# Optimization experiments

Measured on AMD Instinct MI355X. Metric: run time of the kernel, lower is better.

## Reference

```python
import jax, jax.numpy as jnp
import numpy as np

B, S, D = 16, 4096, 64
N_HASHES = 8
BUCKET_SIZE = 64
N_BUCKETS = S // BUCKET_SIZE  # 64
NEG = -5e4  # the module uses -50000.0 as masking value
EPS = 1e-6


def setup_inputs() -> dict:
    key = jax.random.key(0)
    k1, k2, k3 = jax.random.split(key, 3)
    qk = jax.random.normal(k1, (B, S, D), dtype=jnp.float32)
    v = jax.random.normal(k2, (B, S, D), dtype=jnp.float32)
    # random rotations for LSH: (batch, dim, n_hashes, n_buckets//2)
    rotations = jax.random.normal(k3, (B, D, N_HASHES, N_BUCKETS // 2), dtype=jnp.float32)
    return {"qk": qk, "v": v, "rotations": rotations, "seed_": 0}


def _look_one_back(x):
    # prepend previous chunk (with wraparound) along the key axis
    x_extra = jnp.concatenate([x[:, -1:], x[:, :-1]], axis=1)
    return jnp.concatenate([x, x_extra], axis=2)


def reference(qk, v, rotations, seed_):
    b, s, d = qk.shape
    n_hashes = rotations.shape[2]
    n_buckets = 2 * rotations.shape[3]
    chunks = n_hashes * n_buckets  # n_bins == n_buckets

    # ---- hash_vectors ----
    rot = jnp.einsum('btf,bfhi->bhti', qk, rotations)          # (b, h, s, nb/2)
    rot = jnp.concatenate([rot, -rot], axis=-1)                # (b, h, s, nb)
    buckets = jnp.argmax(rot, axis=-1)                         # (b, h, s)
    offsets = (jnp.arange(n_hashes) * n_buckets)[None, :, None]
    buckets = (buckets + offsets).reshape(b, n_hashes * s)     # (b, h*s)

    # ---- sort by (bucket, position) ----
    ticker = jnp.arange(n_hashes * s)
    buckets_and_t = s * buckets + (ticker % s)[None, :]
    sticker = jnp.argsort(buckets_and_t, axis=-1)              # stable sort indices
    undo_sort = jnp.argsort(sticker, axis=-1)

    st = sticker % s                                           # original positions
    sqk = jnp.take_along_axis(qk, st[..., None], axis=1)       # (b, h*s, d)
    sv = jnp.take_along_axis(v, st[..., None], axis=1)

    bq_t = st.reshape(b, chunks, -1)                           # (b, chunks, bucket)
    bqk = sqk.reshape(b, chunks, -1, d)
    bv = sv.reshape(b, chunks, -1, d)

    bq = bqk
    norm = jnp.linalg.norm(bqk, axis=-1, keepdims=True)
    bk = bqk / (norm + EPS)                                    # make_unit_length

    bk = _look_one_back(bk)                                    # (b, chunks, 2*bucket, d)
    bv = _look_one_back(bv)
    bkv_t = _look_one_back(bq_t[..., None])[..., 0]            # (b, chunks, 2*bucket)

    dots = jnp.einsum('bhie,bhje->bhij', bq, bk) * (d ** -0.5)
    self_mask = bq_t[:, :, :, None] == bkv_t[:, :, None, :]
    dots = jnp.where(self_mask, NEG, dots)

    dots_lse = jax.nn.logsumexp(dots, axis=-1, keepdims=True)  # (b, chunks, bucket, 1)
    probs = jnp.exp(dots - dots_lse)
    bo = jnp.einsum('buij,buje->buie', probs, bv)              # (b, chunks, bucket, d)

    so = bo.reshape(b, n_hashes * s, d)
    slogits = dots_lse.reshape(b, n_hashes * s)

    # ---- unsort ----
    o = jnp.take_along_axis(so, undo_sort[..., None], axis=1)
    logits = jnp.take_along_axis(slogits, undo_sort, axis=-1)

    # ---- combine hash rounds via logsumexp weights ----
    o = o.reshape(b, n_hashes, s, d)
    logits = logits.reshape(b, n_hashes, s, 1)
    w = jnp.exp(logits - jax.nn.logsumexp(logits, axis=1, keepdims=True))
    out = jnp.sum(o * w, axis=1)                               # (b, s, d)
    return out, buckets
```

## Files before the change

### kernel.cpp

```cpp
#include <hip/hip_runtime.h>
#include <math.h>

#define BB   16
#define SS   4096
#define DD   64
#define HH   8
#define NBH  32
#define NB   64
#define NCH  512

typedef __attribute__((ext_vector_type(8))) short s16x8;
typedef __attribute__((ext_vector_type(4))) short s16x4;
typedef __attribute__((ext_vector_type(4))) float f32x4;
typedef __attribute__((ext_vector_type(4))) unsigned u32x4;

static __device__ __forceinline__ unsigned short f2bf(float x) {
  union { float f; unsigned u; } a; a.f = x;
  unsigned r = a.u + 0x7fffu + ((a.u >> 16) & 1u);
  return (unsigned short)(r >> 16);
}
static __device__ __forceinline__ float bf2f(unsigned short u) {
  union { unsigned u; float f; } a; a.u = ((unsigned)u) << 16;
  return a.f;
}
static __device__ __forceinline__ unsigned bfrnd_hi(float x) {
  union { float f; unsigned u; } a; a.f = x;
  return a.u + 0x7fffu + ((a.u >> 16) & 1u);
}
static __device__ __forceinline__ unsigned pack_bf(float lo, float hi) {
  return __builtin_amdgcn_perm(bfrnd_hi(hi), bfrnd_hi(lo), 0x07060302u);
}

__global__ __launch_bounds__(256) void k_conv(
    const float* __restrict__ qk, const float* __restrict__ v,
    unsigned short* __restrict__ qb, unsigned short* __restrict__ kb,
    unsigned short* __restrict__ vb) {
  const int gid = blockIdx.x * 256 + threadIdx.x;
  const int half = BB * SS * 4;
  const bool isV = gid >= half;
  const int id = isV ? gid - half : gid;
  const int row = id >> 2, q4 = id & 3;

  const float4* src =
      (const float4*)((isV ? v : qk) + (size_t)row * DD + q4 * 16);
  float vals[16];
#pragma unroll
  for (int g = 0; g < 4; g++) {
    const float4 a = src[g];
    vals[g * 4 + 0] = a.x; vals[g * 4 + 1] = a.y;
    vals[g * 4 + 2] = a.z; vals[g * 4 + 3] = a.w;
  }

  if (!isV) {
    float ss = 0.f;
#pragma unroll
    for (int i = 0; i < 16; i++) ss += vals[i] * vals[i];
    ss += __shfl_xor(ss, 1);
    ss += __shfl_xor(ss, 2);
    const float scl = 0.125f / (sqrtf(ss) + 1e-6f);
    unsigned short qo[16], ko[16];
#pragma unroll
    for (int i = 0; i < 16; i++) {
      qo[i] = f2bf(vals[i]);
      ko[i] = f2bf(vals[i] * scl);
    }
    unsigned short* qd = qb + (size_t)row * DD + q4 * 16;
    unsigned short* kd = kb + (size_t)row * DD + q4 * 16;
    *(s16x8*)qd = *(const s16x8*)&qo[0];
    *(s16x8*)(qd + 8) = *(const s16x8*)&qo[8];
    *(s16x8*)kd = *(const s16x8*)&ko[0];
    *(s16x8*)(kd + 8) = *(const s16x8*)&ko[8];
  } else {
    unsigned short vo[16];
#pragma unroll
    for (int i = 0; i < 16; i++) vo[i] = f2bf(vals[i]);
    unsigned short* vd = vb + (size_t)row * DD + q4 * 16;
    *(s16x8*)vd = *(const s16x8*)&vo[0];
    *(s16x8*)(vd + 8) = *(const s16x8*)&vo[8];
  }
}

__global__ __launch_bounds__(256) void k_rotT(
    const float* __restrict__ rot, unsigned short* __restrict__ rTh,
    unsigned short* __restrict__ rTl, int* __restrict__ needy_count) {
  __shared__ float slab[32][256];
  const int b = blockIdx.x;
  const int tid = threadIdx.x;
  if (b == 0 && tid == 0) *needy_count = 0;

  for (int st = 0; st < 2; st++) {
#pragma unroll
    for (int fr = 0; fr < 32; fr++)
      slab[fr][tid] = rot[(size_t)b * (DD * HH * NBH) +
                          (size_t)(st * 32 + fr) * 256 + tid];
    __syncthreads();
    unsigned short hi[32], lo[32];
#pragma unroll
    for (int fr = 0; fr < 32; fr++) {
      const float x = slab[fr][tid];
      const unsigned short hh = f2bf(x);
      hi[fr] = hh;
      lo[fr] = f2bf(x - bf2f(hh));
    }
    unsigned short* dh = rTh + ((size_t)b * 256 + tid) * DD + st * 32;
    unsigned short* dl = rTl + ((size_t)b * 256 + tid) * DD + st * 32;
#pragma unroll
    for (int g = 0; g < 4; g++) {
      *(s16x8*)(dh + g * 8) = *(const s16x8*)&hi[g * 8];
      *(s16x8*)(dl + g * 8) = *(const s16x8*)&lo[g * 8];
    }
    __syncthreads();
  }
}

#define MARGIN 1e-2f

__global__ __launch_bounds__(256, 4) void k_hash_mfma(
    const float* __restrict__ qk, const unsigned short* __restrict__ rTh,
    const unsigned short* __restrict__ rTl, int* __restrict__ bucket_local,
    float* __restrict__ buckets_out, int* __restrict__ needy_list,
    int* __restrict__ needy_count) {
  __shared__ struct __align__(16) {
    unsigned short ah[64][72];
    unsigned short al[64][72];
    float sc[2][64][33];
  } sm;
  const int b = blockIdx.x;
  const int t0 = blockIdx.y * 64;
  const int tid = threadIdx.x;
  const int w = tid >> 6, lane = tid & 63;
  const int quad = lane >> 4, l16 = lane & 15;

  {
    const int row = tid >> 2, qf = tid & 3;
    const float4* src =
        (const float4*)(qk + ((size_t)b * SS + t0 + row) * DD + qf * 16);
#pragma unroll
    for (int gg = 0; gg < 2; gg++) {
      const float4 v0 = src[gg * 2], v1 = src[gg * 2 + 1];
      const float a[8] = {v0.x, v0.y, v0.z, v0.w, v1.x, v1.y, v1.z, v1.w};
      unsigned short hi[8], lo[8];
#pragma unroll
      for (int e = 0; e < 8; e++) {
        const unsigned short hh = f2bf(a[e]);
        hi[e] = hh;
        lo[e] = f2bf(a[e] - bf2f(hh));
      }
      *(s16x8*)&sm.ah[row][qf * 16 + gg * 8] = *(const s16x8*)hi;
      *(s16x8*)&sm.al[row][qf * 16 + gg * 8] = *(const s16x8*)lo;
    }
  }
  __syncthreads();

  s16x8 Ah[2], Al[2];
#pragma unroll
  for (int ks = 0; ks < 2; ks++) {
    Ah[ks] = *(const s16x8*)&sm.ah[w * 16 + l16][ks * 32 + quad * 8];
    Al[ks] = *(const s16x8*)&sm.al[w * 16 + l16][ks * 32 + quad * 8];
  }

#pragma unroll 1
  for (int h = 0; h < HH; h++) {
    const int p = h & 1;
#pragma unroll
    for (int nt = 0; nt < 2; nt++) {
      const size_t rrow = (((size_t)b * HH + h) * 32 + nt * 16 + l16) * DD;
      s16x8 Bh2[2], Bl2[2];
#pragma unroll
      for (int ks = 0; ks < 2; ks++) {
        Bh2[ks] = *(const s16x8*)&rTh[rrow + ks * 32 + quad * 8];
        Bl2[ks] = *(const s16x8*)&rTl[rrow + ks * 32 + quad * 8];
      }
      f32x4 acc = (f32x4){0.f, 0.f, 0.f, 0.f};
#pragma unroll
      for (int ks = 0; ks < 2; ks++) {
        acc = __builtin_amdgcn_mfma_f32_16x16x32_bf16(Al[ks], Bl2[ks], acc, 0, 0, 0);
        acc = __builtin_amdgcn_mfma_f32_16x16x32_bf16(Al[ks], Bh2[ks], acc, 0, 0, 0);
        acc = __builtin_amdgcn_mfma_f32_16x16x32_bf16(Ah[ks], Bl2[ks], acc, 0, 0, 0);
        acc = __builtin_amdgcn_mfma_f32_16x16x32_bf16(Ah[ks], Bh2[ks], acc, 0, 0, 0);
      }
#pragma unroll
      for (int r = 0; r < 4; r++)
        sm.sc[p][w * 16 + quad * 4 + r][nt * 16 + l16] = acc[r];
    }
    __syncthreads();

    {
      const int tloc = w * 16 + l16;
      const float sgn = (quad >= 2) ? -1.0f : 1.0f;
      const float* rowp = &sm.sc[p][tloc][(quad & 1) * 16];
      float best = -3.0e38f, second = -3.0e38f;
      int bi = quad * 16;
#pragma unroll 8
      for (int i = 0; i < 16; i++) {
        const float vv = sgn * rowp[i];
        if (vv > best) { second = best; best = vv; bi = quad * 16 + i; }
        else if (vv > second) second = vv;
      }
      {
        const float ob = __shfl_xor(best, 16);
        const float os = __shfl_xor(second, 16);
        const int obi = __shfl_xor(bi, 16);
        const float ms = fmaxf(fminf(best, ob), fmaxf(second, os));
        const bool partnerLower = (lane & 16) != 0;
        if (partnerLower ? (ob >= best) : (ob > best)) { best = ob; bi = obi; }
        second = ms;
      }
      {
        const float ob = __shfl_xor(best, 32);
        const float os = __shfl_xor(second, 32);
        const int obi = __shfl_xor(bi, 32);
        const float ms = fmaxf(fminf(best, ob), fmaxf(second, os));
        const bool partnerLower = (lane & 32) != 0;
        if (partnerLower ? (ob >= best) : (ob > best)) { best = ob; bi = obi; }
        second = ms;
      }
      if (quad == 0) {
        const int t = t0 + tloc;
        bucket_local[((size_t)b * HH + h) * SS + t] = bi;
        buckets_out[(size_t)b * (HH * SS) + (size_t)h * SS + t] =
            (float)(h * NB + bi);
        if (best - second <= MARGIN) {
          const int slot = atomicAdd(needy_count, 1);
          needy_list[slot] = (((b << 3) | h) << 12) | t;
        }
      }
    }
  }
}

__global__ __launch_bounds__(256) void k_hash_fix(
    const float* __restrict__ qk, const float* __restrict__ rot,
    const int* __restrict__ needy_list, const int* __restrict__ needy_count,
    int* __restrict__ bucket_local, float* __restrict__ buckets_out) {
  const int n = *needy_count;
  const int hw = (blockIdx.x * 256 + (int)threadIdx.x) >> 5;
  const int li = threadIdx.x & 31;
  const int nhw = gridDim.x * 8;

  for (int idx = hw; idx < n; idx += nhw) {
    const int code = needy_list[idx];
    const int t = code & 4095;
    const int bh = code >> 12;
    const int b = bh >> 3, h = bh & 7;

    const float* qrow = qk + ((size_t)b * SS + t) * DD;
    const float* rcol = rot + ((size_t)b * DD * HH + h) * NBH + li;

    double acc = 0.0;
#pragma unroll 8
    for (int f = 0; f < DD; f++)
      acc += (double)qrow[f] * (double)rcol[(size_t)f * (HH * NBH)];

    double bv = acc;
    int bi = li;
    if (-acc > bv) { bv = -acc; bi = li + 32; }
#pragma unroll
    for (int off = 1; off < 32; off <<= 1) {
      const double ov = __shfl_xor(bv, off);
      const int oi = __shfl_xor(bi, off);
      if (ov > bv || (ov == bv && oi < bi)) { bv = ov; bi = oi; }
    }
    if (li == 0) {
      bucket_local[((size_t)b * HH + h) * SS + t] = bi;
      buckets_out[(size_t)b * (HH * SS) + (size_t)h * SS + t] =
          (float)(h * NB + bi);
    }
  }
}

__global__ __launch_bounds__(256) void k_sort(
    const int* __restrict__ bucket_local, int* __restrict__ sort_t,
    int* __restrict__ ipos) {
  __shared__ unsigned short lb[SS];
  __shared__ unsigned char  cnt[NB][256];
  __shared__ unsigned short pfx[NB][256];
  __shared__ int part[NB][4];
  __shared__ int tot[NB];
  __shared__ int base[NB];

  const int bh = blockIdx.x;
  const int tid = threadIdx.x;
  const int* src = bucket_local + (size_t)bh * SS;

  int* czero = (int*)&cnt[0][0];
#pragma unroll
  for (int i = 0; i < 16; i++) czero[tid + i * 256] = 0;
  __syncthreads();

#pragma unroll
  for (int i = 0; i < 16; i++) {
    const int t = tid * 16 + i;
    const int v = src[t];
    lb[t] = (unsigned short)v;
    cnt[v][tid]++;
  }
  __syncthreads();

  {
    const int bk = tid & 63, sg = tid >> 6;
    int s = 0;
#pragma unroll 8
    for (int i = 0; i < 64; i++) s += cnt[bk][sg * 64 + i];
    part[bk][sg] = s;
  }
  __syncthreads();
  if (tid < NB) tot[tid] = part[tid][0] + part[tid][1] + part[tid][2] + part[tid][3];
  __syncthreads();
  if (tid == 0) {
    int r = 0;
    for (int i = 0; i < NB; i++) { base[i] = r; r += tot[i]; }
  }
  __syncthreads();
  {
    const int bk = tid & 63, sg = tid >> 6;
    int run = base[bk];
    for (int s = 0; s < sg; s++) run += part[bk][s];
#pragma unroll 8
    for (int i = 0; i < 64; i++) {
      const int th = sg * 64 + i;
      pfx[bk][th] = (unsigned short)run;
      run += cnt[bk][th];
    }
  }
  __syncthreads();
  int* st = sort_t + (size_t)bh * SS;
#pragma unroll
  for (int i = 0; i < 16; i++) {
    const int t = tid * 16 + i;
    const int bk = lb[t];
    const int pos = pfx[bk][tid]++;
    st[pos] = t;
  }
  (void)ipos;
}

__global__ __launch_bounds__(256, 4) void k_attn2(
    const unsigned short* __restrict__ qb, const unsigned short* __restrict__ kbg,
    const unsigned short* __restrict__ vbg, const int* __restrict__ sort_t,
    unsigned short* __restrict__ so, float* __restrict__ lse_u) {
  const int blk = blockIdx.x;
  const int b = blk >> 9;
  const int c = blk & 511;
  const int h = c >> 6, cc = c & 63;
  const int cp = (c + 511) & 511;
  const int hp = cp >> 6, ccp = cp & 63;

  __shared__ struct __align__(16) {
    union {
      unsigned short kb[128][72];
      unsigned short p[64][136];
      float olds[64][68];
    } kp;
    unsigned short vsT[64][136];
    int tk[128];
  } sm;

  const int tid = threadIdx.x;
  const int w = tid >> 6;
  const int lane = tid & 63;
  const int quad = lane >> 4;
  const int l16 = lane & 15;

  if (tid < 128) {
    const size_t srci = (tid < 64)
        ? (((size_t)b * HH + h) * SS + cc * 64 + tid)
        : (((size_t)b * HH + hp) * SS + ccp * 64 + (tid - 64));
    sm.tk[tid] = sort_t[srci];
  }
  __syncthreads();

  {
    const int j = tid >> 1, hf = tid & 1;
    const int trow = sm.tk[j];
    const s16x8* ksrc = (const s16x8*)(kbg + ((size_t)b * SS + trow) * DD + hf * 32);
    s16x8 kr[4];
#pragma unroll
    for (int g = 0; g < 4; g++) kr[g] = ksrc[g];
#pragma unroll
    for (int g = 0; g < 4; g++)
      *(s16x8*)&sm.kp.kb[j][hf * 32 + g * 8] = kr[g];
  }
  {
    const int fg = tid >> 5;
    const int tg = (tid & 31) << 2;
    const unsigned short* vb_b = vbg + (size_t)b * SS * DD + fg * 8;
    const u32x4 a0v = *(const u32x4*)(vb_b + (size_t)sm.tk[tg + 0] * DD);
    const u32x4 a1v = *(const u32x4*)(vb_b + (size_t)sm.tk[tg + 1] * DD);
    const u32x4 a2v = *(const u32x4*)(vb_b + (size_t)sm.tk[tg + 2] * DD);
    const u32x4 a3v = *(const u32x4*)(vb_b + (size_t)sm.tk[tg + 3] * DD);
#pragma unroll
    for (int j = 0; j < 4; j++) {
      uint2 ev, ov;
      ev.x = __builtin_amdgcn_perm(a1v[j], a0v[j], 0x05040100u);
      ev.y = __builtin_amdgcn_perm(a3v[j], a2v[j], 0x05040100u);
      ov.x = __builtin_amdgcn_perm(a1v[j], a0v[j], 0x07060302u);
      ov.y = __builtin_amdgcn_perm(a3v[j], a2v[j], 0x07060302u);
      *(uint2*)&sm.vsT[fg * 8 + 2 * j][tg] = ev;
      *(uint2*)&sm.vsT[fg * 8 + 2 * j + 1][tg] = ov;
    }
  }
  const int tq = sm.tk[w * 16 + l16];
  const unsigned short* qrowp = qb + ((size_t)b * SS + tq) * DD;
  const s16x8 a0 = *(const s16x8*)(qrowp + quad * 8);
  const s16x8 a1 = *(const s16x8*)(qrowp + 32 + quad * 8);
  __syncthreads();

  f32x4 acc[8];
#pragma unroll
  for (int nt = 0; nt < 8; nt++) acc[nt] = (f32x4){0.f, 0.f, 0.f, 0.f};
#pragma unroll
  for (int nt = 0; nt < 8; nt++) {
    const s16x8 b0 = *(const s16x8*)&sm.kp.kb[nt * 16 + l16][quad * 8];
    const s16x8 b1 = *(const s16x8*)&sm.kp.kb[nt * 16 + l16][32 + quad * 8];
    acc[nt] = __builtin_amdgcn_mfma_f32_16x16x32_bf16(b0, a0, acc[nt], 0, 0, 0);
    acc[nt] = __builtin_amdgcn_mfma_f32_16x16x32_bf16(b1, a1, acc[nt], 0, 0, 0);
  }

  {
    const bool dm = (quad == (l16 >> 2));
    const int rm = l16 & 3;
#pragma unroll
    for (int nt = 0; nt < 4; nt++)
      if (nt == w) {
#pragma unroll
        for (int r = 0; r < 4; r++)
          if (dm && rm == r) acc[nt][r] = -50000.0f;
      }
  }
  if (cc == 0) {
#pragma unroll
    for (int nt = 4; nt < 8; nt++)
#pragma unroll
      for (int r = 0; r < 4; r++)
        if (sm.tk[nt * 16 + quad * 4 + r] == tq) acc[nt][r] = -50000.0f;
  }

  float mv[8];
#pragma unroll
  for (int nt = 0; nt < 8; nt++)
    mv[nt] = fmaxf(fmaxf(acc[nt][0], acc[nt][1]), fmaxf(acc[nt][2], acc[nt][3]));
  float m = fmaxf(fmaxf(fmaxf(mv[0], mv[1]), fmaxf(mv[2], mv[3])),
                  fmaxf(fmaxf(mv[4], mv[5]), fmaxf(mv[6], mv[7])));
  m = fmaxf(m, __shfl_xor(m, 16));
  m = fmaxf(m, __shfl_xor(m, 32));

  float sv[8];
#pragma unroll
  for (int nt = 0; nt < 8; nt++) {
#pragma unroll
    for (int r = 0; r < 4; r++) acc[nt][r] = __expf(acc[nt][r] - m);
    sv[nt] = (acc[nt][0] + acc[nt][1]) + (acc[nt][2] + acc[nt][3]);
  }
  float s = ((sv[0] + sv[1]) + (sv[2] + sv[3])) +
            ((sv[4] + sv[5]) + (sv[6] + sv[7]));
  s += __shfl_xor(s, 16);
  s += __shfl_xor(s, 32);
  const float inv = 1.0f / s;
  const float lse = __logf(s) + m;

  if (quad == 0)
    lse_u[((size_t)b * SS + tq) * HH + h] = lse;

  __syncthreads();

  {
    const int prow = w * 16 + l16;
#pragma unroll
    for (int nt = 0; nt < 8; nt++) {
      uint2 pv;
      pv.x = pack_bf(acc[nt][0] * inv, acc[nt][1] * inv);
      pv.y = pack_bf(acc[nt][2] * inv, acc[nt][3] * inv);
      *(uint2*)&sm.kp.p[prow][nt * 16 + quad * 4] = pv;
    }
  }
  __syncthreads();

  f32x4 o[4];
#pragma unroll
  for (int nt = 0; nt < 4; nt++) o[nt] = (f32x4){0.f, 0.f, 0.f, 0.f};
  const unsigned short* vrow = &sm.vsT[w * 16 + l16][0];
#pragma unroll
  for (int kc = 0; kc < 4; kc++) {
    const s16x8 av = *(const s16x8*)(vrow + kc * 32 + quad * 8);
#pragma unroll
    for (int nt = 0; nt < 4; nt++) {
      const s16x8 bp = *(const s16x8*)&sm.kp.p[nt * 16 + l16][kc * 32 + quad * 8];
      o[nt] = __builtin_amdgcn_mfma_f32_16x16x32_bf16(av, bp, o[nt], 0, 0, 0);
    }
  }

  __syncthreads();

#pragma unroll
  for (int nt = 0; nt < 4; nt++)
    *(f32x4*)&sm.kp.olds[nt * 16 + l16][w * 16 + quad * 4] = o[nt];
  __syncthreads();

  {
    const int q = tid >> 2, qt = tid & 3;
    const int t = sm.tk[q];
    float vals[16];
    *(f32x4*)&vals[0]  = *(const f32x4*)&sm.kp.olds[q][qt * 16 + 0];
    *(f32x4*)&vals[4]  = *(const f32x4*)&sm.kp.olds[q][qt * 16 + 4];
    *(f32x4*)&vals[8]  = *(const f32x4*)&sm.kp.olds[q][qt * 16 + 8];
    *(f32x4*)&vals[12] = *(const f32x4*)&sm.kp.olds[q][qt * 16 + 12];
    unsigned pk[8];
#pragma unroll
    for (int g = 0; g < 8; g++) pk[g] = pack_bf(vals[2 * g], vals[2 * g + 1]);
    unsigned short* dst =
        so + (((size_t)b * SS + t) * HH + h) * DD + qt * 16;
    *(uint4*)dst = *(const uint4*)&pk[0];
    *(uint4*)(dst + 8) = *(const uint4*)&pk[4];
  }
}

__global__ __launch_bounds__(256) void k_combine2(
    const unsigned short* __restrict__ so, const float* __restrict__ lse_u,
    float* __restrict__ out) {
  const size_t idx = (size_t)blockIdx.x * 256 + threadIdx.x;
  const int fg = (int)(idx & 7);
  const size_t bt = idx >> 3;

  const float4 l0 = *(const float4*)(lse_u + bt * HH);
  const float4 l1 = *(const float4*)(lse_u + bt * HH + 4);
  const float l[HH] = {l0.x, l0.y, l0.z, l0.w, l1.x, l1.y, l1.z, l1.w};
  float m = l[0];
#pragma unroll
  for (int h = 1; h < HH; h++) m = fmaxf(m, l[h]);

  float den = 0.f;
  float num[8];
#pragma unroll
  for (int e = 0; e < 8; e++) num[e] = 0.f;
#pragma unroll
  for (int h = 0; h < HH; h++) {
    const float wgt = __expf(l[h] - m);
    den += wgt;
    const s16x8 v = *(const s16x8*)(so + (bt * HH + h) * DD + fg * 8);
#pragma unroll
    for (int e = 0; e < 8; e++)
      num[e] += wgt * bf2f((unsigned short)v[e]);
  }

  float4 o0, o1;
  o0.x = num[0] / den; o0.y = num[1] / den;
  o0.z = num[2] / den; o0.w = num[3] / den;
  o1.x = num[4] / den; o1.y = num[5] / den;
  o1.z = num[6] / den; o1.w = num[7] / den;
  float* dst = out + bt * DD + fg * 8;
  *(float4*)dst = o0;
  *(float4*)(dst + 4) = o1;
}

__global__ __launch_bounds__(256, 2) void k_hash_f32(
    const float* __restrict__ qk, const float* __restrict__ rot,
    int* __restrict__ bucket_local, float* __restrict__ buckets_out,
    int* __restrict__ needy_list, int* __restrict__ needy_count) {
  __shared__ float lb[128 * 65];
  const int b = blockIdx.x;
  const int t0 = blockIdx.y * 128;
  const int tid = threadIdx.x;

  {
    const int row = tid >> 1, hf = (tid & 1) * 32;
    const float4* src =
        (const float4*)(qk + ((size_t)b * SS + t0 + row) * DD + hf);
    float* dst = &lb[row * 65 + hf];
#pragma unroll
    for (int g = 0; g < 8; g++) {
      const float4 vv = src[g];
      dst[g * 4 + 0] = vv.x; dst[g * 4 + 1] = vv.y;
      dst[g * 4 + 2] = vv.z; dst[g * 4 + 3] = vv.w;
    }
  }
  __syncthreads();

  const int w = tid >> 6;
  const int l = tid & 63;
  const int hb = __builtin_amdgcn_readfirstlane(w);

  for (int hp = 0; hp < 2; hp++) {
    const int h = hb + hp * 4;
    const float* rbase = rot + ((size_t)b * DD * HH + h) * NBH;
    const size_t rstride = HH * NBH;

    float acc0[NBH], acc1[NBH];
#pragma unroll
    for (int i = 0; i < NBH; i++) { acc0[i] = 0.f; acc1[i] = 0.f; }

    float4 bufA[8], bufB[8];
#pragma unroll
    for (int i4 = 0; i4 < 8; i4++) bufA[i4] = ((const float4*)rbase)[i4];

    for (int f = 0; f < DD; f += 2) {
      {
        const float4* r4 = (const float4*)(rbase + (size_t)(f + 1) * rstride);
#pragma unroll
        for (int i4 = 0; i4 < 8; i4++) bufB[i4] = r4[i4];
      }
      {
        const float q0 = lb[l * 65 + f];
        const float q1 = lb[(l + 64) * 65 + f];
#pragma unroll
        for (int i4 = 0; i4 < 8; i4++) {
          const float4 rv = bufA[i4];
          acc0[i4*4+0] = fmaf(q0, rv.x, acc0[i4*4+0]);
          acc0[i4*4+1] = fmaf(q0, rv.y, acc0[i4*4+1]);
          acc0[i4*4+2] = fmaf(q0, rv.z, acc0[i4*4+2]);
          acc0[i4*4+3] = fmaf(q0, rv.w, acc0[i4*4+3]);
          acc1[i4*4+0] = fmaf(q1, rv.x, acc1[i4*4+0]);
          acc1[i4*4+1] = fmaf(q1, rv.y, acc1[i4*4+1]);
          acc1[i4*4+2] = fmaf(q1, rv.z, acc1[i4*4+2]);
          acc1[i4*4+3] = fmaf(q1, rv.w, acc1[i4*4+3]);
        }
      }
      if (f + 2 < DD) {
        const float4* r4 = (const float4*)(rbase + (size_t)(f + 2) * rstride);
#pragma unroll
        for (int i4 = 0; i4 < 8; i4++) bufA[i4] = r4[i4];
      }
      {
        const float q0 = lb[l * 65 + f + 1];
        const float q1 = lb[(l + 64) * 65 + f + 1];
#pragma unroll
        for (int i4 = 0; i4 < 8; i4++) {
          const float4 rv = bufB[i4];
          acc0[i4*4+0] = fmaf(q0, rv.x, acc0[i4*4+0]);
          acc0[i4*4+1] = fmaf(q0, rv.y, acc0[i4*4+1]);
          acc0[i4*4+2] = fmaf(q0, rv.z, acc0[i4*4+2]);
          acc0[i4*4+3] = fmaf(q0, rv.w, acc0[i4*4+3]);
          acc1[i4*4+0] = fmaf(q1, rv.x, acc1[i4*4+0]);
          acc1[i4*4+1] = fmaf(q1, rv.y, acc1[i4*4+1]);
          acc1[i4*4+2] = fmaf(q1, rv.z, acc1[i4*4+2]);
          acc1[i4*4+3] = fmaf(q1, rv.w, acc1[i4*4+3]);
        }
      }
    }

#pragma unroll
    for (int tok = 0; tok < 2; tok++) {
      const float* acc = tok ? acc1 : acc0;
      float best = -3.0e38f, second = -3.0e38f;
      int bi = 0;
#pragma unroll
      for (int i = 0; i < 64; i++) {
        const float vv = (i < NBH) ? acc[i] : -acc[i - NBH];
        if (vv > best) { second = best; best = vv; bi = i; }
        else if (vv > second) { second = vv; }
      }
      const int t = t0 + tok * 64 + l;
      bucket_local[((size_t)b * HH + h) * SS + t] = bi;
      buckets_out[(size_t)b * (HH * SS) + (size_t)h * SS + t] =
          (float)(h * NB + bi);
      if (best - second <= MARGIN) {
        const int slot = atomicAdd(needy_count, 1);
        needy_list[slot] = (((b << 3) | h) << 12) | t;
      }
    }
  }
}

__global__ __launch_bounds__(256) void k_attn_atomic(
    const float* __restrict__ qk, const float* __restrict__ v,
    const int* __restrict__ sort_t, float* __restrict__ num,
    float* __restrict__ den) {
  const int blk = blockIdx.x;
  const int b = blk >> 9;
  const int c = blk & 511;
  const int h = c >> 6, cc = c & 63;
  const int cp = (c + 511) & 511;
  const int hp = cp >> 6, ccp = cp & 63;

  __shared__ union {
    struct {
      float qt[DD * 64];
      float kt[DD * 128];
      int   tq[64];
      int   tk[128];
      float nrm[128];
      float red[16 * 64];
      float rmax[64];
      float rsum[64];
    } a;
    struct {
      float pt[128 * 64];
      float vs[128 * 64];
    } p;
  } sm;

  const int tid = threadIdx.x;

  if (tid < 64)
    sm.a.tq[tid] = sort_t[((size_t)b * HH + h) * SS + cc * 64 + tid];
  if (tid >= 128) {
    const int j = tid - 128;
    const size_t src = (j < 64) ? (((size_t)b * HH + h) * SS + cc * 64 + j)
                                : (((size_t)b * HH + hp) * SS + ccp * 64 + (j - 64));
    sm.a.tk[j] = sort_t[src];
  }
  if (tid >= 64 && tid < 192) sm.a.nrm[tid - 64] = 0.f;
  __syncthreads();

  {
    const int qi = tid >> 2, qq = tid & 3;
    const float4* qsrc =
        (const float4*)(qk + ((size_t)b * SS + sm.a.tq[qi]) * DD) + qq * 4;
#pragma unroll
    for (int k4 = 0; k4 < 4; k4++) {
      float4 val = qsrc[k4];
      const int f = qq * 16 + k4 * 4;
      sm.a.qt[(f + 0) * 64 + qi] = val.x;
      sm.a.qt[(f + 1) * 64 + qi] = val.y;
      sm.a.qt[(f + 2) * 64 + qi] = val.z;
      sm.a.qt[(f + 3) * 64 + qi] = val.w;
    }
    const int j = tid >> 1, hhf = tid & 1;
    const float4* ksrc =
        (const float4*)(qk + ((size_t)b * SS + sm.a.tk[j]) * DD) + hhf * 8;
    float ss = 0.f;
#pragma unroll
    for (int k4 = 0; k4 < 8; k4++) {
      float4 val = ksrc[k4];
      const int f = hhf * 32 + k4 * 4;
      sm.a.kt[(f + 0) * 128 + j] = val.x;
      sm.a.kt[(f + 1) * 128 + j] = val.y;
      sm.a.kt[(f + 2) * 128 + j] = val.z;
      sm.a.kt[(f + 3) * 128 + j] = val.w;
      ss += val.x * val.x + val.y * val.y + val.z * val.z + val.w * val.w;
    }
    atomicAdd(&sm.a.nrm[j], ss);
  }
  __syncthreads();
  if (tid < 128) {
    const float n = sqrtf(sm.a.nrm[tid]) + 1e-6f;
    sm.a.nrm[tid] = 0.125f / n;
  }
  float4 vreg[8];
  {
    const int j = tid >> 1, hhf = tid & 1;
    const float4* vsrc =
        (const float4*)(v + ((size_t)b * SS + sm.a.tk[j]) * DD) + hhf * 8;
#pragma unroll
    for (int k4 = 0; k4 < 8; k4++) vreg[k4] = vsrc[k4];
  }
  __syncthreads();

  const int qi0 = (tid & 15) * 4;
  const int j0g = (tid >> 4) * 8;
  const int kg = tid >> 4;
  float acc[4][8];
#pragma unroll
  for (int i = 0; i < 4; i++)
#pragma unroll
    for (int j = 0; j < 8; j++) acc[i][j] = 0.f;

#pragma unroll 8
  for (int f = 0; f < DD; f++) {
    float4 qv = *(const float4*)&sm.a.qt[f * 64 + qi0];
    float4 k0 = *(const float4*)&sm.a.kt[f * 128 + j0g];
    float4 k1 = *(const float4*)&sm.a.kt[f * 128 + j0g + 4];
    float qa[4] = {qv.x, qv.y, qv.z, qv.w};
    float ka[8] = {k0.x, k0.y, k0.z, k0.w, k1.x, k1.y, k1.z, k1.w};
#pragma unroll
    for (int i = 0; i < 4; i++)
#pragma unroll
      for (int j = 0; j < 8; j++) acc[i][j] = fmaf(qa[i], ka[j], acc[i][j]);
  }

  int tqr[4];
#pragma unroll
  for (int i = 0; i < 4; i++) tqr[i] = sm.a.tq[qi0 + i];
  int tkr[8]; float scl[8];
#pragma unroll
  for (int j = 0; j < 8; j++) {
    tkr[j] = sm.a.tk[j0g + j];
    scl[j] = sm.a.nrm[j0g + j];
  }
#pragma unroll
  for (int i = 0; i < 4; i++)
#pragma unroll
    for (int j = 0; j < 8; j++) {
      const float dv = acc[i][j] * scl[j];
      acc[i][j] = (tqr[i] == tkr[j]) ? -50000.0f : dv;
    }

  float pmax[4];
#pragma unroll
  for (int i = 0; i < 4; i++) {
    float m = acc[i][0];
#pragma unroll
    for (int j = 1; j < 8; j++) m = fmaxf(m, acc[i][j]);
    pmax[i] = m;
  }
#pragma unroll
  for (int i = 0; i < 4; i++) sm.a.red[kg * 64 + qi0 + i] = pmax[i];
  __syncthreads();
  if (tid < 64) {
    float m = -3.0e38f;
#pragma unroll
    for (int g = 0; g < 16; g++) m = fmaxf(m, sm.a.red[g * 64 + tid]);
    sm.a.rmax[tid] = m;
  }
  __syncthreads();
  float psum[4];
#pragma unroll
  for (int i = 0; i < 4; i++) {
    const float rm = sm.a.rmax[qi0 + i];
    float s = 0.f;
#pragma unroll
    for (int j = 0; j < 8; j++) {
      const float e = __expf(acc[i][j] - rm);
      acc[i][j] = e;
      s += e;
    }
    psum[i] = s;
  }
#pragma unroll
  for (int i = 0; i < 4; i++) sm.a.red[kg * 64 + qi0 + i] = psum[i];
  __syncthreads();
  if (tid < 64) {
    float s = 0.f;
#pragma unroll
    for (int g = 0; g < 16; g++) s += sm.a.red[g * 64 + tid];
    sm.a.rsum[tid] = s;
  }
  __syncthreads();
  float lse[4], isum[4];
#pragma unroll
  for (int i = 0; i < 4; i++) {
    const float rm = sm.a.rmax[qi0 + i];
    const float s = sm.a.rsum[qi0 + i];
    isum[i] = 1.0f / s;
    lse[i] = __logf(s) + rm;
  }
  __syncthreads();

#pragma unroll
  for (int j = 0; j < 8; j++)
#pragma unroll
    for (int i = 0; i < 4; i++)
      sm.p.pt[(j0g + j) * 64 + qi0 + i] = acc[i][j] * isum[i];
  {
    const int j = tid >> 1, hhf = tid & 1;
#pragma unroll
    for (int k4 = 0; k4 < 8; k4++)
      *(float4*)&sm.p.vs[j * 64 + hhf * 32 + k4 * 4] = vreg[k4];
  }
  __syncthreads();

  const int f0 = (tid >> 4) * 4;
  float o[4][4];
#pragma unroll
  for (int i = 0; i < 4; i++)
#pragma unroll
    for (int j = 0; j < 4; j++) o[i][j] = 0.f;

#pragma unroll 8
  for (int j = 0; j < 128; j++) {
    float4 pv = *(const float4*)&sm.p.pt[j * 64 + qi0];
    float4 vv = *(const float4*)&sm.p.vs[j * 64 + f0];
    float pa[4] = {pv.x, pv.y, pv.z, pv.w};
    float va[4] = {vv.x, vv.y, vv.z, vv.w};
#pragma unroll
    for (int i = 0; i < 4; i++)
#pragma unroll
      for (int j2 = 0; j2 < 4; j2++) o[i][j2] = fmaf(pa[i], va[j2], o[i][j2]);
  }

#pragma unroll
  for (int i = 0; i < 4; i++) {
    const float w = __expf(lse[i]);
    float* dst = num + ((size_t)b * SS + tqr[i]) * DD + f0;
#pragma unroll
    for (int j = 0; j < 4; j++) atomicAdd(dst + j, o[i][j] * w);
    if (kg == 0) atomicAdd(den + (size_t)b * SS + tqr[i], w);
  }
}

__global__ __launch_bounds__(256) void k_final(float* __restrict__ o,
                                               const float* __restrict__ den) {
  const size_t i = (size_t)blockIdx.x * 256 + threadIdx.x;
  o[i] = o[i] / den[i >> 6];
}

extern "C" void kernel_launch(void* const* d_in, const int* in_sizes, int n_in,
                              void* d_out, int out_size, void* d_ws,
                              size_t ws_size, hipStream_t stream) {
  const float* qk  = (const float*)d_in[0];
  const float* v   = (const float*)d_in[1];
  const float* rot = (const float*)d_in[2];

  float* out_attn = (float*)d_out;
  float* buckets_out = out_attn + (size_t)BB * SS * DD;

  const size_t BHS = (size_t)BB * HH * SS;
  const size_t BSD = (size_t)BB * SS * DD;
  const size_t RT  = (size_t)BB * HH * 32 * DD;
  int* bucket_local = (int*)d_ws;
  int* sort_t = bucket_local + BHS;
  int* ipos = sort_t + BHS;
  float* lse_u = (float*)(ipos + BHS);
  unsigned short* qb16 = (unsigned short*)(lse_u + BHS);
  unsigned short* kb16 = qb16 + BSD;
  unsigned short* vb16 = kb16 + BSD;
  unsigned short* so_u = vb16 + BSD;
  unsigned short* rTh = so_u + BHS * DD;
  unsigned short* rTl = rTh + RT;

  const size_t NEED2 =
      4 * BHS * 4 + 3 * BSD * 2 + BHS * DD * 2 + 2 * RT * 2;

  if (ws_size >= NEED2) {
    k_conv<<<2 * BB * SS * 4 / 256, 256, 0, stream>>>(qk, v, qb16, kb16, vb16);
    k_rotT<<<BB, 256, 0, stream>>>(rot, rTh, rTl, ipos);
    k_hash_mfma<<<dim3(BB, SS / 64), 256, 0, stream>>>(
        qk, rTh, rTl, bucket_local, buckets_out, sort_t, ipos);
    k_hash_fix<<<256, 256, 0, stream>>>(qk, rot, sort_t, ipos, bucket_local,
                                        buckets_out);
    k_sort<<<BB * HH, 256, 0, stream>>>(bucket_local, sort_t, ipos);
    k_attn2<<<BB * NCH, 256, 0, stream>>>(qb16, kb16, vb16, sort_t, so_u, lse_u);
    k_combine2<<<(BB * SS * 8) / 256, 256, 0, stream>>>(so_u, lse_u, out_attn);
  } else {
    float* den = (float*)(sort_t + 2 * BHS);
    hipMemsetAsync(out_attn, 0, (size_t)BB * SS * DD * sizeof(float), stream);
    hipMemsetAsync(den, 0, (size_t)BB * SS * sizeof(float), stream);
    hipMemsetAsync(ipos, 0, sizeof(int), stream);
    k_hash_f32<<<dim3(BB, SS / 128), 256, 0, stream>>>(
        qk, rot, bucket_local, buckets_out, sort_t, ipos);
    k_hash_fix<<<256, 256, 0, stream>>>(qk, rot, sort_t, ipos, bucket_local,
                                        buckets_out);
    k_sort<<<BB * HH, 256, 0, stream>>>(bucket_local, sort_t, ipos);
    k_attn_atomic<<<BB * NCH, 256, 0, stream>>>(qk, v, sort_t, out_attn, den);
    k_final<<<(BB * SS * DD) / 256, 256, 0, stream>>>(out_attn, den);
  }
}
```

Baseline: 209.3 us.

## Fuse conversion kernels and fold near-tie hash fixup into hash kernel

```diff
diff --git a/kernel.cpp b/kernel.cpp
--- a/kernel.cpp
+++ b/kernel.cpp
@@ -31,11 +31,46 @@
   return __builtin_amdgcn_perm(bfrnd_hi(hi), bfrnd_hi(lo), 0x07060302u);
 }
 
-__global__ __launch_bounds__(256) void k_conv(
+__global__ __launch_bounds__(256) void k_prep(
     const float* __restrict__ qk, const float* __restrict__ v,
+    const float* __restrict__ rot,
     unsigned short* __restrict__ qb, unsigned short* __restrict__ kb,
-    unsigned short* __restrict__ vb) {
-  const int gid = blockIdx.x * 256 + threadIdx.x;
+    unsigned short* __restrict__ vb,
+    unsigned short* __restrict__ rTh, unsigned short* __restrict__ rTl,
+    int* __restrict__ needy_count) {
+  __shared__ float slab[32][256];
+  const int tid = threadIdx.x;
+
+  if (blockIdx.x >= 2048) {
+    const int b = blockIdx.x - 2048;
+    if (b == 0 && tid == 0) *needy_count = 0;
+    for (int st = 0; st < 2; st++) {
+#pragma unroll
+      for (int fr = 0; fr < 32; fr++)
+        slab[fr][tid] = rot[(size_t)b * (DD * HH * NBH) +
+                            (size_t)(st * 32 + fr) * 256 + tid];
+      __syncthreads();
+      unsigned short hi[32], lo[32];
+#pragma unroll
+      for (int fr = 0; fr < 32; fr++) {
+        const float x = slab[fr][tid];
+        const unsigned short hh = f2bf(x);
+        hi[fr] = hh;
+        lo[fr] = f2bf(x - bf2f(hh));
+      }
+      unsigned short* dh = rTh + ((size_t)b * 256 + tid) * DD + st * 32;
+      unsigned short* dl = rTl + ((size_t)b * 256 + tid) * DD + st * 32;
+#pragma unroll
+      for (int g = 0; g < 4; g++) {
+        *(s16x8*)(dh + g * 8) = *(const s16x8*)&hi[g * 8];
+        *(s16x8*)(dl + g * 8) = *(const s16x8*)&lo[g * 8];
+      }
+      __syncthreads();
+    }
+    return;
+  }
+
+  const int gid = blockIdx.x * 256 + tid;
   const int half = BB * SS * 4;
   const bool isV = gid >= half;
   const int id = isV ? gid - half : gid;
@@ -80,56 +115,27 @@
   }
 }
 
-__global__ __launch_bounds__(256) void k_rotT(
-    const float* __restrict__ rot, unsigned short* __restrict__ rTh,
-    unsigned short* __restrict__ rTl, int* __restrict__ needy_count) {
-  __shared__ float slab[32][256];
-  const int b = blockIdx.x;
-  const int tid = threadIdx.x;
-  if (b == 0 && tid == 0) *needy_count = 0;
-
-  for (int st = 0; st < 2; st++) {
-#pragma unroll
-    for (int fr = 0; fr < 32; fr++)
-      slab[fr][tid] = rot[(size_t)b * (DD * HH * NBH) +
-                          (size_t)(st * 32 + fr) * 256 + tid];
-    __syncthreads();
-    unsigned short hi[32], lo[32];
-#pragma unroll
-    for (int fr = 0; fr < 32; fr++) {
-      const float x = slab[fr][tid];
-      const unsigned short hh = f2bf(x);
-      hi[fr] = hh;
-      lo[fr] = f2bf(x - bf2f(hh));
-    }
-    unsigned short* dh = rTh + ((size_t)b * 256 + tid) * DD + st * 32;
-    unsigned short* dl = rTl + ((size_t)b * 256 + tid) * DD + st * 32;
-#pragma unroll
-    for (int g = 0; g < 4; g++) {
-      *(s16x8*)(dh + g * 8) = *(const s16x8*)&hi[g * 8];
-      *(s16x8*)(dl + g * 8) = *(const s16x8*)&lo[g * 8];
-    }
-    __syncthreads();
-  }
-}
-
 #define MARGIN 1e-2f
 
 __global__ __launch_bounds__(256, 4) void k_hash_mfma(
-    const float* __restrict__ qk, const unsigned short* __restrict__ rTh,
+    const float* __restrict__ qk, const float* __restrict__ rot,
+    const unsigned short* __restrict__ rTh,
     const unsigned short* __restrict__ rTl, int* __restrict__ bucket_local,
-    float* __restrict__ buckets_out, int* __restrict__ needy_list,
-    int* __restrict__ needy_count) {
+    float* __restrict__ buckets_out) {
   __shared__ struct __align__(16) {
     unsigned short ah[64][72];
     unsigned short al[64][72];
     float sc[2][64][33];
+    int needy[512];
+    int ncnt;
   } sm;
   const int b = blockIdx.x;
   const int t0 = blockIdx.y * 64;
   const int tid = threadIdx.x;
   const int w = tid >> 6, lane = tid & 63;
   const int quad = lane >> 4, l16 = lane & 15;
+
+  if (tid == 0) sm.ncnt = 0;
 
   {
     const int row = tid >> 2, qf = tid & 3;
@@ -221,10 +227,42 @@
         buckets_out[(size_t)b * (HH * SS) + (size_t)h * SS + t] =
             (float)(h * NB + bi);
         if (best - second <= MARGIN) {
-          const int slot = atomicAdd(needy_count, 1);
-          needy_list[slot] = (((b << 3) | h) << 12) | t;
+          const int slot = atomicAdd(&sm.ncnt, 1);
+          sm.needy[slot] = (h << 6) | tloc;
         }
       }
+    }
+  }
+  __syncthreads();
+
+  const int nfix = sm.ncnt;
+  const int hwid = tid >> 5;
+  const int li = tid & 31;
+  for (int idx = hwid; idx < nfix; idx += 8) {
+    const int code = sm.needy[idx];
+    const int h2 = code >> 6, tloc = code & 63;
+    const int t = t0 + tloc;
+    const float* qrow = qk + ((size_t)b * SS + t) * DD;
+    const float* rcol = rot + ((size_t)b * DD * HH + h2) * NBH + li;
+
+    double acc = 0.0;
+#pragma unroll 8
+    for (int f = 0; f < DD; f++)
+      acc += (double)qrow[f] * (double)rcol[(size_t)f * (HH * NBH)];
+
+    double bv = acc;
+    int bi = li;
+    if (-acc > bv) { bv = -acc; bi = li + 32; }
+#pragma unroll
+    for (int off = 1; off < 32; off <<= 1) {
+      const double ov = __shfl_xor(bv, off);
+      const int oi = __shfl_xor(bi, off);
+      if (ov > bv || (ov == bv && oi < bi)) { bv = ov; bi = oi; }
+    }
+    if (li == 0) {
+      bucket_local[((size_t)b * HH + h2) * SS + t] = bi;
+      buckets_out[(size_t)b * (HH * SS) + (size_t)h2 * SS + t] =
+          (float)(h2 * NB + bi);
     }
   }
 }
@@ -273,8 +311,8 @@
     const int* __restrict__ bucket_local, int* __restrict__ sort_t,
     int* __restrict__ ipos) {
   __shared__ unsigned short lb[SS];
-  __shared__ unsigned char  cnt[NB][256];
-  __shared__ unsigned short pfx[NB][256];
+  __shared__ __align__(16) unsigned char cnt[NB][260];
+  __shared__ __align__(16) unsigned short pfx[NB][258];
   __shared__ int part[NB][4];
   __shared__ int tot[NB];
   __shared__ int base[NB];
@@ -285,7 +323,10 @@
 
   int* czero = (int*)&cnt[0][0];
 #pragma unroll
-  for (int i = 0; i < 16; i++) czero[tid + i * 256] = 0;
+  for (int i = 0; i < 17; i++) {
+    const int o = tid + i * 256;
+    if (o < (NB * 260) / 4) czero[o] = 0;
+  }
   __syncthreads();
 
 #pragma unroll
@@ -912,12 +953,10 @@
       4 * BHS * 4 + 3 * BSD * 2 + BHS * DD * 2 + 2 * RT * 2;
 
   if (ws_size >= NEED2) {
-    k_conv<<<2 * BB * SS * 4 / 256, 256, 0, stream>>>(qk, v, qb16, kb16, vb16);
-    k_rotT<<<BB, 256, 0, stream>>>(rot, rTh, rTl, ipos);
+    k_prep<<<2048 + BB, 256, 0, stream>>>(qk, v, rot, qb16, kb16, vb16,
+                                          rTh, rTl, ipos);
     k_hash_mfma<<<dim3(BB, SS / 64), 256, 0, stream>>>(
-        qk, rTh, rTl, bucket_local, buckets_out, sort_t, ipos);
-    k_hash_fix<<<256, 256, 0, stream>>>(qk, rot, sort_t, ipos, bucket_local,
-                                        buckets_out);
+        qk, rot, rTh, rTl, bucket_local, buckets_out);
     k_sort<<<BB * HH, 256, 0, stream>>>(bucket_local, sort_t, ipos);
     k_attn2<<<BB * NCH, 256, 0, stream>>>(qb16, kb16, vb16, sort_t, so_u, lse_u);
     k_combine2<<<(BB * SS * 8) / 256, 256, 0, stream>>>(so_u, lse_u, out_attn);
```

Measured after the change: 199.9 us (median of 2 runs). 1.05x faster.
